# Kernel tuning notes

Measured on AMD Instinct MI355X. Metric: run time of the kernel, lower is better.

The kernel has to match this reference:

```python
import jax, jax.numpy as jnp
import numpy as np

# LLaMA-7B style BitNet b1.58 MLP dims
B, S = 2, 2048
H, I = 4096, 11008
EPS = 1e-8
QMAX = 127.0  # int8 activation range


def _ternary_weight(key, shape):
    """BitNet b1.58 absmean weight quantization: per-tensor scale, ternary {-1,0,1}."""
    w = jax.random.normal(key, shape, jnp.float32) * 0.02
    ws = jnp.mean(jnp.abs(w)) + EPS
    qw = jnp.clip(jnp.round(w / ws), -1.0, 1.0)
    return qw, ws


def setup_inputs() -> dict:
    key = jax.random.key(0)
    k0, k1, k2, k3 = jax.random.split(key, 4)
    # x arrives already absmean-quantized to int8 values (stored as float) + scalar scale
    xf = jax.random.normal(k0, (B, S, H), jnp.float32)
    xs = jnp.mean(jnp.abs(xf)) + EPS
    x = jnp.clip(jnp.round(xf / xs), -QMAX - 1, QMAX)
    qw_gate, ws_gate = _ternary_weight(k1, (I, H))
    qw_up, ws_up = _ternary_weight(k2, (I, H))
    qw_down, ws_down = _ternary_weight(k3, (H, I))
    return {"x": x, "x_scale": xs,
            "qw_gate": qw_gate, "ws_gate": ws_gate,
            "qw_up": qw_up, "ws_up": ws_up,
            "qw_down": qw_down, "ws_down": ws_down}


def absmean_quantize(x):
    """Per-tensor absmean quantization to int8 range with straight-through rounding."""
    scale = jnp.mean(jnp.abs(x)) + EPS
    c = x / scale
    q = c + jax.lax.stop_gradient(jnp.clip(jnp.round(c), -QMAX - 1, QMAX) - c)
    return q, scale


def quantized_linear(xq, xs, qw, ws):
    # integer-valued GEMM; output scale is product of input and weight scales
    out = jnp.einsum('bsh,ih->bsi', xq, qw)
    return out, xs * ws


def reference(x, x_scale, qw_gate, ws_gate, qw_up, ws_up, qw_down, ws_down):
    gate, gate_s = quantized_linear(x, x_scale, qw_gate, ws_gate)      # [B,S,I]
    up, up_s = quantized_linear(x, x_scale, qw_up, ws_up)              # [B,S,I]
    # quantized_act: dequant -> SiLU -> re-quantize (absmean)
    ga_q, ga_s = absmean_quantize(jax.nn.silu(gate * gate_s))
    # quantized elementwise matmul: multiply q-values, multiply scales, re-quantize
    inter_q, inter_s = absmean_quantize(ga_q * up * (ga_s * up_s))
    # down projection (I -> H): einsum over intermediate dim
    out = jnp.einsum('bsi,hi->bsh', inter_q, qw_down)
    return out, inter_s * ws_down
```

## Files before the change

### kernel.cpp

```cpp
#include <hip/hip_runtime.h>
#include <math.h>

#define TOK 4096
#define HD  4096
#define ID  11008

typedef int i32x4 __attribute__((ext_vector_type(4)));
typedef float f32x4v __attribute__((ext_vector_type(4)));
typedef char i8x4v __attribute__((ext_vector_type(4)));

#define GLDS16(g, l) __builtin_amdgcn_global_load_lds( \
    (const __attribute__((address_space(1))) void*)(g), \
    (__attribute__((address_space(3))) void*)(l), 16, 0, 0)

__global__ void conv_all(const float* __restrict__ x,  char* __restrict__ xq,
                         const float* __restrict__ wg, char* __restrict__ wgq,
                         const float* __restrict__ wu, char* __restrict__ wuq,
                         const float* __restrict__ wd, char* __restrict__ wdq)
{
  const long NX = (long)TOK * HD / 4, NW = (long)ID * HD / 4;
  const long total = NX + 3 * NW;
  const long stride = (long)gridDim.x * blockDim.x;
  for (long i = (long)blockIdx.x * blockDim.x + threadIdx.x; i < total;
       i += stride) {
    const f32x4v* src; i8x4v* dst; long j;
    if (i < NX)               { src = (const f32x4v*)x;  dst = (i8x4v*)xq;  j = i; }
    else if (i < NX + NW)     { src = (const f32x4v*)wg; dst = (i8x4v*)wgq; j = i - NX; }
    else if (i < NX + 2 * NW) { src = (const f32x4v*)wu; dst = (i8x4v*)wuq; j = i - NX - NW; }
    else                      { src = (const f32x4v*)wd; dst = (i8x4v*)wdq; j = i - NX - 2 * NW; }
    f32x4v v = __builtin_nontemporal_load(&src[j]);
    i8x4v o;
    o.x = (char)(int)rintf(v.x);
    o.y = (char)(int)rintf(v.y);
    o.z = (char)(int)rintf(v.z);
    o.w = (char)(int)rintf(v.w);
    dst[j] = o;
  }
}

template<int MODE>
__global__ __launch_bounds__(256, 4)
void gemm_i8(const char* __restrict__ A,
             const char* __restrict__ Bm,
             int M, int N, int K,
             float* __restrict__ Cout,
             const float* __restrict__ ga_in,
             const float* __restrict__ sc0,
             const float* __restrict__ sc1,
             double* __restrict__ sums,
             long long NN)
{
  __shared__ char As[16384];
  __shared__ char Bs[16384];

  const int tid  = threadIdx.x;
  const int w    = tid >> 6;
  const int lane = tid & 63;
  const int wr   = lane & 15;
  const int qd   = lane >> 4;
  const int wm   = (w >> 1) << 6;
  const int wn   = (w & 1) << 6;

  const int L   = blockIdx.y * gridDim.x + blockIdx.x;
  const int xcd = L & 7;
  const int r   = L >> 3;
  const int m0  = (xcd + ((r & 3) << 3)) << 7;
  const int n0  = (r >> 2) << 7;

  i32x4 acc[4][4] = {};

  const int rowL = tid >> 3;
  const int chk  = (tid & 7) ^ (rowL & 7);
  const char* gA = A  + (size_t)(m0 + rowL) * K + (chk << 4);
  const char* gB = Bm + (size_t)(n0 + rowL) * K + (chk << 4);
  const size_t rk32 = (size_t)32 * K;
  char* lA = As + (w << 10);
  char* lB = Bs + (w << 10);

  const int s7    = wr & 7;
  const int abase = ((wm + wr) << 7) + ((qd ^ s7) << 4);
  const int bbase = ((wn + wr) << 7) + ((qd ^ s7) << 4);

  for (int k0 = 0; k0 < K; k0 += 128) {
    GLDS16(gA + k0,            lA);
    GLDS16(gA + k0 +     rk32, lA + 4096);
    GLDS16(gA + k0 + 2 * rk32, lA + 8192);
    GLDS16(gA + k0 + 3 * rk32, lA + 12288);
    GLDS16(gB + k0,            lB);
    GLDS16(gB + k0 +     rk32, lB + 4096);
    GLDS16(gB + k0 + 2 * rk32, lB + 8192);
    GLDS16(gB + k0 + 3 * rk32, lB + 12288);
    __syncthreads();

#pragma unroll
    for (int h = 0; h < 2; h++) {
      const int hx = h << 6;
      i32x4 af[4], bfr[4];
#pragma unroll
      for (int i = 0; i < 4; i++)
        af[i] = *(const i32x4*)(As + ((abase + (i << 11)) ^ hx));
#pragma unroll
      for (int j = 0; j < 4; j++)
        bfr[j] = *(const i32x4*)(Bs + ((bbase + (j << 11)) ^ hx));

#pragma unroll
      for (int i = 0; i < 4; i++)
#pragma unroll
        for (int j = 0; j < 4; j++)
          acc[i][j] = __builtin_amdgcn_mfma_i32_16x16x64_i8(af[i], bfr[j],
                                                            acc[i][j], 0, 0, 0);
    }
    __syncthreads();
  }

  double lsum = 0.0;

  if (MODE == 0) {
    const float gs = sc0[0] * sc1[0];
#pragma unroll
    for (int i = 0; i < 4; i++) {
      const int mb = m0 + wm + (i << 4) + (qd << 2);
#pragma unroll
      for (int j = 0; j < 4; j++) {
        const int n = n0 + wn + (j << 4) + wr;
#pragma unroll
        for (int r2 = 0; r2 < 4; r2++) {
          float g = (float)acc[i][j][r2] * gs;
          float s = g / (1.0f + expf(-g));
          __builtin_nontemporal_store(s, &Cout[(size_t)(mb + r2) * N + n]);
          lsum += (double)fabsf(s);
        }
      }
    }
  } else if (MODE == 1) {
    const float up_s  = sc0[0] * sc1[0];
    const float ga_s  = (float)(sums[0] / (double)NN) + 1e-8f;
    const float combo = ga_s * up_s;
#pragma unroll
    for (int i = 0; i < 4; i++) {
      const int mb = m0 + wm + (i << 4) + (qd << 2);
#pragma unroll
      for (int j = 0; j < 4; j++) {
        const int n = n0 + wn + (j << 4) + wr;
#pragma unroll
        for (int r2 = 0; r2 < 4; r2++) {
          float up = (float)acc[i][j][r2];
          float ga = __builtin_nontemporal_load(
                         &ga_in[(size_t)(mb + r2) * N + n]);
          float gq = fmaxf(-128.0f, fminf(127.0f, rintf(ga / ga_s)));
          float itv = gq * up * combo;
          __builtin_nontemporal_store(itv, &Cout[(size_t)(mb + r2) * N + n]);
          lsum += (double)fabsf(itv);
        }
      }
    }
  } else {
#pragma unroll
    for (int i = 0; i < 4; i++) {
      const int mb = m0 + wm + (i << 4) + (qd << 2);
#pragma unroll
      for (int j = 0; j < 4; j++) {
        const int n = n0 + wn + (j << 4) + wr;
#pragma unroll
        for (int r2 = 0; r2 < 4; r2++)
          __builtin_nontemporal_store((float)acc[i][j][r2],
                                      &Cout[(size_t)(mb + r2) * N + n]);
      }
    }
  }

  if (MODE != 2) {
    for (int off = 32; off; off >>= 1) lsum += __shfl_down(lsum, off, 64);
    double* red = (double*)As;
    if (lane == 0) red[w] = lsum;
    __syncthreads();
    if (tid == 0) atomicAdd(&sums[MODE], red[0] + red[1] + red[2] + red[3]);
  }
}

__global__ void quant_inter(const float* __restrict__ inter,
                            char* __restrict__ outq,
                            const double* __restrict__ sums, long long NN,
                            const float* __restrict__ wsd,
                            float* __restrict__ scalar_out, int n4)
{
  const float is = (float)(sums[1] / (double)NN) + 1e-8f;
  if (blockIdx.x == 0 && threadIdx.x == 0) scalar_out[0] = is * wsd[0];
  int stride = gridDim.x * blockDim.x;
  for (int i = blockIdx.x * blockDim.x + threadIdx.x; i < n4; i += stride) {
    f32x4v v = __builtin_nontemporal_load(&((const f32x4v*)inter)[i]);
    i8x4v o;
    o.x = (char)(int)fmaxf(-128.0f, fminf(127.0f, rintf(v.x / is)));
    o.y = (char)(int)fmaxf(-128.0f, fminf(127.0f, rintf(v.y / is)));
    o.z = (char)(int)fmaxf(-128.0f, fminf(127.0f, rintf(v.z / is)));
    o.w = (char)(int)fmaxf(-128.0f, fminf(127.0f, rintf(v.w / is)));
    ((i8x4v*)outq)[i] = o;
  }
}

extern "C" void kernel_launch(void* const* d_in, const int* in_sizes, int n_in,
                              void* d_out, int out_size, void* d_ws, size_t ws_size,
                              hipStream_t stream) {
  const float* x        = (const float*)d_in[0];
  const float* x_scale  = (const float*)d_in[1];
  const float* qw_gate  = (const float*)d_in[2];
  const float* ws_gate  = (const float*)d_in[3];
  const float* qw_up    = (const float*)d_in[4];
  const float* ws_up    = (const float*)d_in[5];
  const float* qw_down  = (const float*)d_in[6];
  const float* ws_down  = (const float*)d_in[7];
  float* out = (float*)d_out;

  char* ws = (char*)d_ws;
  double* sums = (double*)ws;
  size_t off = 256;
  char* xq     = ws + off; off += (size_t)TOK * HD;
  char* wgq    = ws + off; off += (size_t)ID * HD;
  char* wuq    = ws + off; off += (size_t)ID * HD;
  char* wdq    = ws + off; off += (size_t)HD * ID;
  char* interq = ws + off; off += (size_t)TOK * ID;
  float* ga    = (float*)(ws + off); off += (size_t)TOK * ID * 4;
  float* inter = (float*)(ws + off); off += (size_t)TOK * ID * 4;

  const long long NN = (long long)TOK * ID;

  (void)hipMemsetAsync(sums, 0, 16, stream);

  conv_all<<<8192, 256, 0, stream>>>(x, xq, qw_gate, wgq, qw_up, wuq,
                                     qw_down, wdq);

  gemm_i8<0><<<dim3(ID / 128, TOK / 128), 256, 0, stream>>>(
      xq, wgq, TOK, ID, HD, ga, nullptr, x_scale, ws_gate, sums, NN);

  gemm_i8<1><<<dim3(ID / 128, TOK / 128), 256, 0, stream>>>(
      xq, wuq, TOK, ID, HD, inter, ga, x_scale, ws_up, sums, NN);

  quant_inter<<<8192, 256, 0, stream>>>(inter, interq, sums, NN, ws_down,
                                        out + (size_t)TOK * HD, (int)(NN / 4));

  gemm_i8<2><<<dim3(HD / 128, TOK / 128), 256, 0, stream>>>(
      interq, wdq, TOK, HD, ID, out, nullptr, nullptr, nullptr, sums, NN);
}
```

Before: 1.106 ms.

## Fuse gate and up GEMMs into one kernel sharing A tiles

```diff
diff --git a/kernel.cpp b/kernel.cpp
--- a/kernel.cpp
+++ b/kernel.cpp
@@ -38,17 +38,125 @@
   }
 }
 
-template<int MODE>
+__global__ __launch_bounds__(256, 2)
+void gemm_gateup(const char* __restrict__ A,
+                 const char* __restrict__ Bg,
+                 const char* __restrict__ Bu,
+                 int M, int N, int K,
+                 float* __restrict__ gaOut,
+                 float* __restrict__ upOut,
+                 const float* __restrict__ sc0,
+                 const float* __restrict__ sc1,
+                 double* __restrict__ sums)
+{
+  __shared__ char As[16384];
+  __shared__ char Bgs[16384];
+  __shared__ char Bus[16384];
+
+  const int tid  = threadIdx.x;
+  const int w    = tid >> 6;
+  const int lane = tid & 63;
+  const int wr   = lane & 15;
+  const int qd   = lane >> 4;
+  const int wm   = (w >> 1) << 6;
+  const int wn   = (w & 1) << 6;
+
+  const int L   = blockIdx.y * gridDim.x + blockIdx.x;
+  const int xcd = L & 7;
+  const int r   = L >> 3;
+  const int m0  = (xcd + ((r & 3) << 3)) << 7;
+  const int n0  = (r >> 2) << 7;
+
+  i32x4 accg[4][4] = {};
+  i32x4 accu[4][4] = {};
+
+  const int rowL = tid >> 3;
+  const int chk  = (tid & 7) ^ (rowL & 7);
+  const char* gA  = A  + (size_t)(m0 + rowL) * K + (chk << 4);
+  const char* gBg = Bg + (size_t)(n0 + rowL) * K + (chk << 4);
+  const char* gBu = Bu + (size_t)(n0 + rowL) * K + (chk << 4);
+  const size_t rk32 = (size_t)32 * K;
+  char* lA  = As  + (w << 10);
+  char* lBg = Bgs + (w << 10);
+  char* lBu = Bus + (w << 10);
+
+  const int s7    = wr & 7;
+  const int abase = ((wm + wr) << 7) + ((qd ^ s7) << 4);
+  const int bbase = ((wn + wr) << 7) + ((qd ^ s7) << 4);
+
+  for (int k0 = 0; k0 < K; k0 += 128) {
+    GLDS16(gA + k0,             lA);
+    GLDS16(gA + k0 +     rk32,  lA + 4096);
+    GLDS16(gA + k0 + 2 * rk32,  lA + 8192);
+    GLDS16(gA + k0 + 3 * rk32,  lA + 12288);
+    GLDS16(gBg + k0,            lBg);
+    GLDS16(gBg + k0 +     rk32, lBg + 4096);
+    GLDS16(gBg + k0 + 2 * rk32, lBg + 8192);
+    GLDS16(gBg + k0 + 3 * rk32, lBg + 12288);
+    GLDS16(gBu + k0,            lBu);
+    GLDS16(gBu + k0 +     rk32, lBu + 4096);
+    GLDS16(gBu + k0 + 2 * rk32, lBu + 8192);
+    GLDS16(gBu + k0 + 3 * rk32, lBu + 12288);
+    __syncthreads();
+
+#pragma unroll
+    for (int h = 0; h < 2; h++) {
+      const int hx = h << 6;
+      i32x4 af[4], bg[4], bu[4];
+#pragma unroll
+      for (int i = 0; i < 4; i++)
+        af[i] = *(const i32x4*)(As + ((abase + (i << 11)) ^ hx));
+#pragma unroll
+      for (int j = 0; j < 4; j++) {
+        bg[j] = *(const i32x4*)(Bgs + ((bbase + (j << 11)) ^ hx));
+        bu[j] = *(const i32x4*)(Bus + ((bbase + (j << 11)) ^ hx));
+      }
+
+#pragma unroll
+      for (int i = 0; i < 4; i++)
+#pragma unroll
+        for (int j = 0; j < 4; j++) {
+          accg[i][j] = __builtin_amdgcn_mfma_i32_16x16x64_i8(af[i], bg[j],
+                                                             accg[i][j], 0, 0, 0);
+          accu[i][j] = __builtin_amdgcn_mfma_i32_16x16x64_i8(af[i], bu[j],
+                                                             accu[i][j], 0, 0, 0);
+        }
+    }
+    __syncthreads();
+  }
+
+  double lsum = 0.0;
+  const float gs = sc0[0] * sc1[0];
+#pragma unroll
+  for (int i = 0; i < 4; i++) {
+    const int mb = m0 + wm + (i << 4) + (qd << 2);
+#pragma unroll
+    for (int j = 0; j < 4; j++) {
+      const int n = n0 + wn + (j << 4) + wr;
+#pragma unroll
+      for (int r2 = 0; r2 < 4; r2++) {
+        const size_t idx = (size_t)(mb + r2) * N + n;
+        float g = (float)accg[i][j][r2] * gs;
+        float s = g / (1.0f + expf(-g));
+        __builtin_nontemporal_store(s, &gaOut[idx]);
+        lsum += (double)fabsf(s);
+        __builtin_nontemporal_store((float)accu[i][j][r2], &upOut[idx]);
+      }
+    }
+  }
+
+  for (int off = 32; off; off >>= 1) lsum += __shfl_down(lsum, off, 64);
+  double* red = (double*)As;
+  if (lane == 0) red[w] = lsum;
+  __syncthreads();
+  if (tid == 0) atomicAdd(&sums[0], red[0] + red[1] + red[2] + red[3]);
+}
+
 __global__ __launch_bounds__(256, 4)
-void gemm_i8(const char* __restrict__ A,
-             const char* __restrict__ Bm,
-             int M, int N, int K,
-             float* __restrict__ Cout,
-             const float* __restrict__ ga_in,
-             const float* __restrict__ sc0,
-             const float* __restrict__ sc1,
-             double* __restrict__ sums,
-             long long NN)
+void gemm_i8_down(const char* __restrict__ A,
+                  const char* __restrict__ Bm,
+                  int M, int N, int K,
+                  float* __restrict__ Cout)
 {
   __shared__ char As[16384];
   __shared__ char Bs[16384];
@@ -113,69 +221,51 @@
     __syncthreads();
   }
 
+#pragma unroll
+  for (int i = 0; i < 4; i++) {
+    const int mb = m0 + wm + (i << 4) + (qd << 2);
+#pragma unroll
+    for (int j = 0; j < 4; j++) {
+      const int n = n0 + wn + (j << 4) + wr;
+#pragma unroll
+      for (int r2 = 0; r2 < 4; r2++)
+        __builtin_nontemporal_store((float)acc[i][j][r2],
+                                    &Cout[(size_t)(mb + r2) * N + n]);
+    }
+  }
+}
+
+__global__ void inter_pass(const float* __restrict__ ga,
+                           float* __restrict__ upinter,
+                           const float* __restrict__ xs,
+                           const float* __restrict__ wsu,
+                           double* __restrict__ sums,
+                           long long NN, int n4)
+{
+  const float up_s  = xs[0] * wsu[0];
+  const float ga_s  = (float)(sums[0] / (double)NN) + 1e-8f;
+  const float combo = ga_s * up_s;
   double lsum = 0.0;
-
-  if (MODE == 0) {
-    const float gs = sc0[0] * sc1[0];
-#pragma unroll
-    for (int i = 0; i < 4; i++) {
-      const int mb = m0 + wm + (i << 4) + (qd << 2);
-#pragma unroll
-      for (int j = 0; j < 4; j++) {
-        const int n = n0 + wn + (j << 4) + wr;
-#pragma unroll
-        for (int r2 = 0; r2 < 4; r2++) {
-          float g = (float)acc[i][j][r2] * gs;
-          float s = g / (1.0f + expf(-g));
-          __builtin_nontemporal_store(s, &Cout[(size_t)(mb + r2) * N + n]);
-          lsum += (double)fabsf(s);
-        }
-      }
-    }
-  } else if (MODE == 1) {
-    const float up_s  = sc0[0] * sc1[0];
-    const float ga_s  = (float)(sums[0] / (double)NN) + 1e-8f;
-    const float combo = ga_s * up_s;
-#pragma unroll
-    for (int i = 0; i < 4; i++) {
-      const int mb = m0 + wm + (i << 4) + (qd << 2);
-#pragma unroll
-      for (int j = 0; j < 4; j++) {
-        const int n = n0 + wn + (j << 4) + wr;
-#pragma unroll
-        for (int r2 = 0; r2 < 4; r2++) {
-          float up = (float)acc[i][j][r2];
-          float ga = __builtin_nontemporal_load(
-                         &ga_in[(size_t)(mb + r2) * N + n]);
-          float gq = fmaxf(-128.0f, fminf(127.0f, rintf(ga / ga_s)));
-          float itv = gq * up * combo;
-          __builtin_nontemporal_store(itv, &Cout[(size_t)(mb + r2) * N + n]);
-          lsum += (double)fabsf(itv);
-        }
-      }
-    }
-  } else {
-#pragma unroll
-    for (int i = 0; i < 4; i++) {
-      const int mb = m0 + wm + (i << 4) + (qd << 2);
-#pragma unroll
-      for (int j = 0; j < 4; j++) {
-        const int n = n0 + wn + (j << 4) + wr;
-#pragma unroll
-        for (int r2 = 0; r2 < 4; r2++)
-          __builtin_nontemporal_store((float)acc[i][j][r2],
-                                      &Cout[(size_t)(mb + r2) * N + n]);
-      }
-    }
-  }
-
-  if (MODE != 2) {
-    for (int off = 32; off; off >>= 1) lsum += __shfl_down(lsum, off, 64);
-    double* red = (double*)As;
-    if (lane == 0) red[w] = lsum;
-    __syncthreads();
-    if (tid == 0) atomicAdd(&sums[MODE], red[0] + red[1] + red[2] + red[3]);
-  }
+  const int stride = gridDim.x * blockDim.x;
+  for (int i = blockIdx.x * blockDim.x + threadIdx.x; i < n4; i += stride) {
+    f32x4v gv = __builtin_nontemporal_load(&((const f32x4v*)ga)[i]);
+    f32x4v uv = *(&((f32x4v*)upinter)[i]);
+    f32x4v o;
+#pragma unroll
+    for (int c = 0; c < 4; c++) {
+      float gq  = fmaxf(-128.0f, fminf(127.0f, rintf(gv[c] / ga_s)));
+      float itv = gq * uv[c] * combo;
+      o[c] = itv;
+      lsum += (double)fabsf(itv);
+    }
+    ((f32x4v*)upinter)[i] = o;
+  }
+  for (int off = 32; off; off >>= 1) lsum += __shfl_down(lsum, off, 64);
+  __shared__ double red[4];
+  const int w = threadIdx.x >> 6;
+  if ((threadIdx.x & 63) == 0) red[w] = lsum;
+  __syncthreads();
+  if (threadIdx.x == 0) atomicAdd(&sums[1], red[0] + red[1] + red[2] + red[3]);
 }
 
 __global__ void quant_inter(const float* __restrict__ inter,
@@ -229,15 +319,15 @@
   conv_all<<<8192, 256, 0, stream>>>(x, xq, qw_gate, wgq, qw_up, wuq,
                                      qw_down, wdq);
 
-  gemm_i8<0><<<dim3(ID / 128, TOK / 128), 256, 0, stream>>>(
-      xq, wgq, TOK, ID, HD, ga, nullptr, x_scale, ws_gate, sums, NN);
-
-  gemm_i8<1><<<dim3(ID / 128, TOK / 128), 256, 0, stream>>>(
-      xq, wuq, TOK, ID, HD, inter, ga, x_scale, ws_up, sums, NN);
+  gemm_gateup<<<dim3(ID / 128, TOK / 128), 256, 0, stream>>>(
+      xq, wgq, wuq, TOK, ID, HD, ga, inter, x_scale, ws_gate, sums);
+
+  inter_pass<<<2048, 256, 0, stream>>>(ga, inter, x_scale, ws_up, sums, NN,
+                                       (int)(NN / 4));
 
   quant_inter<<<8192, 256, 0, stream>>>(inter, interq, sums, NN, ws_down,
                                         out + (size_t)TOK * HD, (int)(NN / 4));
 
-  gemm_i8<2><<<dim3(HD / 128, TOK / 128), 256, 0, stream>>>(
-      interq, wdq, TOK, HD, ID, out, nullptr, nullptr, nullptr, sums, NN);
-}
+  gemm_i8_down<<<dim3(HD / 128, TOK / 128), 256, 0, stream>>>(
+      interq, wdq, TOK, HD, ID, out);
+}
```

Result: slower. 1.170 ms (+5.8%).

## Double-buffer int8 GEMM K-loop with 64-wide stages and async prefetch

Applied to the files above, without the earlier changes.

```diff
diff --git a/kernel.cpp b/kernel.cpp
--- a/kernel.cpp
+++ b/kernel.cpp
@@ -39,7 +39,7 @@
 }
 
 template<int MODE>
-__global__ __launch_bounds__(256, 4)
+__global__ __launch_bounds__(256, 3)
 void gemm_i8(const char* __restrict__ A,
              const char* __restrict__ Bm,
              int M, int N, int K,
@@ -69,49 +69,57 @@
 
   i32x4 acc[4][4] = {};
 
-  const int rowL = tid >> 3;
-  const int chk  = (tid & 7) ^ (rowL & 7);
-  const char* gA = A  + (size_t)(m0 + rowL) * K + (chk << 4);
-  const char* gB = Bm + (size_t)(n0 + rowL) * K + (chk << 4);
-  const size_t rk32 = (size_t)32 * K;
-  char* lA = As + (w << 10);
-  char* lB = Bs + (w << 10);
-
-  const int s7    = wr & 7;
-  const int abase = ((wm + wr) << 7) + ((qd ^ s7) << 4);
-  const int bbase = ((wn + wr) << 7) + ((qd ^ s7) << 4);
-
-  for (int k0 = 0; k0 < K; k0 += 128) {
-    GLDS16(gA + k0,            lA);
-    GLDS16(gA + k0 +     rk32, lA + 4096);
-    GLDS16(gA + k0 + 2 * rk32, lA + 8192);
-    GLDS16(gA + k0 + 3 * rk32, lA + 12288);
-    GLDS16(gB + k0,            lB);
-    GLDS16(gB + k0 +     rk32, lB + 4096);
-    GLDS16(gB + k0 + 2 * rk32, lB + 8192);
-    GLDS16(gB + k0 + 3 * rk32, lB + 12288);
-    __syncthreads();
-
-#pragma unroll
-    for (int h = 0; h < 2; h++) {
-      const int hx = h << 6;
-      i32x4 af[4], bfr[4];
-#pragma unroll
-      for (int i = 0; i < 4; i++)
-        af[i] = *(const i32x4*)(As + ((abase + (i << 11)) ^ hx));
+  const int srow = tid >> 2;
+  const int sc   = (tid & 3) ^ ((tid >> 3) & 3);
+  const char* gA = A  + (size_t)(m0 + srow) * K + (sc << 4);
+  const char* gB = Bm + (size_t)(n0 + srow) * K + (sc << 4);
+  const size_t r64K = (size_t)64 * K;
+  char* dA = As + (w << 10);
+  char* dB = Bs + (w << 10);
+
+  const int rsw   = (qd ^ ((wr >> 1) & 3)) << 4;
+  const int abase = ((wm + wr) << 6) + rsw;
+  const int bbase = ((wn + wr) << 6) + rsw;
+
+  const int NH = K >> 6;
+
+#define STAGE(kh) do { const size_t ko = (size_t)(kh) << 6;                \
+    const int hb_ = ((kh) & 1) << 13;                                      \
+    GLDS16(gA + ko,        dA + hb_);                                      \
+    GLDS16(gA + ko + r64K, dA + hb_ + 4096);                               \
+    GLDS16(gB + ko,        dB + hb_);                                      \
+    GLDS16(gB + ko + r64K, dB + hb_ + 4096); } while (0)
+
+  STAGE(0);
+
+#pragma unroll 2
+  for (int kh = 0; kh < NH; ++kh) {
+    if (kh + 1 < NH) {
+      STAGE(kh + 1);
+      asm volatile("s_waitcnt vmcnt(4)" ::: "memory");
+    } else {
+      asm volatile("s_waitcnt vmcnt(0)" ::: "memory");
+    }
+    __builtin_amdgcn_s_barrier();
+
+    const int hb = (kh & 1) << 13;
+    i32x4 af[4], bf[4];
+#pragma unroll
+    for (int i = 0; i < 4; i++)
+      af[i] = *(const i32x4*)(As + hb + abase + (i << 10));
+#pragma unroll
+    for (int j = 0; j < 4; j++)
+      bf[j] = *(const i32x4*)(Bs + hb + bbase + (j << 10));
+
+#pragma unroll
+    for (int i = 0; i < 4; i++)
 #pragma unroll
       for (int j = 0; j < 4; j++)
-        bfr[j] = *(const i32x4*)(Bs + ((bbase + (j << 11)) ^ hx));
-
-#pragma unroll
-      for (int i = 0; i < 4; i++)
-#pragma unroll
-        for (int j = 0; j < 4; j++)
-          acc[i][j] = __builtin_amdgcn_mfma_i32_16x16x64_i8(af[i], bfr[j],
-                                                            acc[i][j], 0, 0, 0);
-    }
-    __syncthreads();
-  }
+        acc[i][j] = __builtin_amdgcn_mfma_i32_16x16x64_i8(af[i], bf[j],
+                                                          acc[i][j], 0, 0, 0);
+    __builtin_amdgcn_s_barrier();
+  }
+#undef STAGE
 
   double lsum = 0.0;
 
```

After: 1.337 ms. +20.9%, slower.
